# Optimization experiments

Measured on AMD Instinct MI355X. Metric: run time of the kernel, lower is better.

Reference implementation:

```python
import jax, jax.numpy as jnp
import numpy as np
from jax.lax import associative_scan

D_H = 512

def _binary_operator(e_i, e_j):
    a_i, kv_i = e_i
    a_j, kv_j = e_j
    return (a_j * a_i, a_j * kv_i + kv_j)

def setup_inputs() -> dict:
    key = jax.random.key(0)
    x = jax.random.normal(key, (4, 8192, 3 * D_H), dtype=jnp.float32)
    return {"x": x}

def reference(x):
    d_h = x.shape[-1] // 3
    inp = jnp.tanh(x[:, :, :d_h])
    gates = jax.nn.sigmoid(x[:, :, d_h:])
    input_gate, output_gate = jnp.split(gates, 2, axis=-1)
    forget_gate = 1.0 - input_gate
    # diagonal linear recurrence h_t = f_t * h_{t-1} + i_t * x_t via associative scan
    _, hidden_state = associative_scan(_binary_operator, (forget_gate, inp * input_gate), axis=1)
    return jnp.tanh(hidden_state) * output_gate
```

## Files before the change

kernel.cpp:

```cpp
#include <hip/hip_runtime.h>


#define B_    4
#define T_    8192
#define DH_   512
#define ROW4_ 384
#define DG4_  128
#define C_    512
#define TC_   (T_ / C_)

typedef float nat4 __attribute__((ext_vector_type(4)));

__device__ __forceinline__ float sigmoid_f(float x) {
    return __fdividef(1.0f, 1.0f + __expf(-x));
}
__device__ __forceinline__ float tanh_f(float x) {
    return 1.0f - __fdividef(2.0f, __expf(2.0f * x) + 1.0f);
}

__device__ __forceinline__ void step_agg(float xv, float gv, float& A, float& K) {
    const float s  = sigmoid_f(gv);
    const float f  = 1.0f - s;
    A = f * A;
    K = f * K + tanh_f(xv) * s;
}

__global__ __launch_bounds__(128) void k_partials(
        const float4* __restrict__ x4,
        float4* __restrict__ aggA,
        float4* __restrict__ aggKV) {
    const int c  = blockIdx.x;
    const int b  = blockIdx.y;
    const int d4 = threadIdx.x;
    const float4* xb = x4 + (size_t)b * T_ * ROW4_;
    const int t0 = c * TC_;

    float4 A  = make_float4(1.0f, 1.0f, 1.0f, 1.0f);
    float4 KV = make_float4(0.0f, 0.0f, 0.0f, 0.0f);
#pragma unroll 4
    for (int i = 0; i < TC_; ++i) {
        const size_t r = (size_t)(t0 + i) * ROW4_ + d4;
        const float4 xi = xb[r];
        const float4 gi = xb[r + DG4_];
        step_agg(xi.x, gi.x, A.x, KV.x);
        step_agg(xi.y, gi.y, A.y, KV.y);
        step_agg(xi.z, gi.z, A.z, KV.z);
        step_agg(xi.w, gi.w, A.w, KV.w);
    }
    const size_t idx = ((size_t)b * C_ + c) * DG4_ + d4;
    aggA[idx]  = A;
    aggKV[idx] = KV;
}

__global__ __launch_bounds__(128) void k_scan(
        const float4* __restrict__ aggA,
        const float4* __restrict__ aggKV,
        float4* __restrict__ pref) {
    const int b  = blockIdx.x;
    const int d4 = threadIdx.x;

    float4 h = make_float4(0.0f, 0.0f, 0.0f, 0.0f);
    for (int c = 0; c < C_; ++c) {
        const size_t idx = ((size_t)b * C_ + c) * DG4_ + d4;
        pref[idx] = h;
        const float4 a  = aggA[idx];
        const float4 kv = aggKV[idx];
        h.x = a.x * h.x + kv.x;
        h.y = a.y * h.y + kv.y;
        h.z = a.z * h.z + kv.z;
        h.w = a.w * h.w + kv.w;
    }
}

__global__ __launch_bounds__(128) void k_apply(
        const float4* __restrict__ x4,
        const float4* __restrict__ pref,
        float4* __restrict__ out4) {
    const int c  = blockIdx.x;
    const int b  = blockIdx.y;
    const int d4 = threadIdx.x;

    float4 h = pref[((size_t)b * C_ + c) * DG4_ + d4];

    const float4* xb = x4 + (size_t)b * T_ * ROW4_;
    float4* ob = out4 + (size_t)b * T_ * DG4_;
    const int t0 = c * TC_;

#pragma unroll 4
    for (int i = 0; i < TC_; ++i) {
        const size_t r = (size_t)(t0 + i) * ROW4_ + d4;
        const float4 xi = xb[r];
        const float4 gi = xb[r + DG4_];
        const float4 go = xb[r + 2 * DG4_];
        float4 o;
        {
            const float s = sigmoid_f(gi.x), f = 1.0f - s;
            h.x = f * h.x + tanh_f(xi.x) * s;
            o.x = tanh_f(h.x) * sigmoid_f(go.x);
        }
        {
            const float s = sigmoid_f(gi.y), f = 1.0f - s;
            h.y = f * h.y + tanh_f(xi.y) * s;
            o.y = tanh_f(h.y) * sigmoid_f(go.y);
        }
        {
            const float s = sigmoid_f(gi.z), f = 1.0f - s;
            h.z = f * h.z + tanh_f(xi.z) * s;
            o.z = tanh_f(h.z) * sigmoid_f(go.z);
        }
        {
            const float s = sigmoid_f(gi.w), f = 1.0f - s;
            h.w = f * h.w + tanh_f(xi.w) * s;
            o.w = tanh_f(h.w) * sigmoid_f(go.w);
        }
        nat4 ov = {o.x, o.y, o.z, o.w};
        __builtin_nontemporal_store(ov, (nat4*)&ob[(size_t)(t0 + i) * DG4_ + d4]);
    }
}

extern "C" void kernel_launch(void* const* d_in, const int* in_sizes, int n_in,
                              void* d_out, int out_size, void* d_ws, size_t ws_size,
                              hipStream_t stream) {
    const float4* x4 = (const float4*)d_in[0];
    float4* out4 = (float4*)d_out;

    float4* aggA  = (float4*)d_ws;
    float4* aggKV = aggA  + (size_t)B_ * C_ * DG4_;
    float4* pref  = aggKV + (size_t)B_ * C_ * DG4_;

    hipLaunchKernelGGL(k_partials, dim3(C_, B_), dim3(128), 0, stream, x4, aggA, aggKV);
    hipLaunchKernelGGL(k_scan,     dim3(B_),     dim3(128), 0, stream, aggA, aggKV, pref);
    hipLaunchKernelGGL(k_apply,    dim3(C_, B_), dim3(128), 0, stream, x4, pref, out4);
}
```

Before: 363.2 us.

## Fuse three-pass chunked scan into one cooperative kernel with two-level prefix

Replaces the partials, serial scan and apply kernels with a single cooperative kernel using grid-wide syncs. Chunk count drops to 256, and the serial per-batch scan over all chunks becomes a two-level scheme: 32 groups scan their chunks locally, then each block combines the preceding group totals. The intent is to remove the long serial scan kernel and the launch gaps between kernels. In exchange it depends on co-residency of all 1024 blocks for grid sync, lowers parallelism per pass, and drops the nontemporal output store.

```diff
diff --git a/kernel.cpp b/kernel.cpp
--- a/kernel.cpp
+++ b/kernel.cpp
@@ -1,15 +1,17 @@
 #include <hip/hip_runtime.h>
+#include <hip/hip_cooperative_groups.h>
+
+namespace cg = cooperative_groups;
 
 
 #define B_    4
 #define T_    8192
-#define DH_   512
 #define ROW4_ 384
 #define DG4_  128
-#define C_    512
+#define C_    256
 #define TC_   (T_ / C_)
-
-typedef float nat4 __attribute__((ext_vector_type(4)));
+#define G_    32
+#define GS_   (C_ / G_)
 
 __device__ __forceinline__ float sigmoid_f(float x) {
     return __fdividef(1.0f, 1.0f + __expf(-x));
@@ -19,73 +21,90 @@
 }
 
 __device__ __forceinline__ void step_agg(float xv, float gv, float& A, float& K) {
-    const float s  = sigmoid_f(gv);
-    const float f  = 1.0f - s;
+    const float s = sigmoid_f(gv);
+    const float f = 1.0f - s;
     A = f * A;
     K = f * K + tanh_f(xv) * s;
 }
 
-__global__ __launch_bounds__(128) void k_partials(
+__device__ __forceinline__ void affine4(float4& h, const float4 a, const float4 kv) {
+    h.x = a.x * h.x + kv.x;
+    h.y = a.y * h.y + kv.y;
+    h.z = a.z * h.z + kv.z;
+    h.w = a.w * h.w + kv.w;
+}
+
+__global__ __launch_bounds__(128, 4) void scan_coop(
         const float4* __restrict__ x4,
+        float4* __restrict__ out4,
         float4* __restrict__ aggA,
-        float4* __restrict__ aggKV) {
+        float4* __restrict__ aggKV,
+        float4* __restrict__ locA,
+        float4* __restrict__ locKV,
+        float4* __restrict__ grpA,
+        float4* __restrict__ grpKV) {
     const int c  = blockIdx.x;
     const int b  = blockIdx.y;
     const int d4 = threadIdx.x;
     const float4* xb = x4 + (size_t)b * T_ * ROW4_;
     const int t0 = c * TC_;
+    cg::grid_group grid = cg::this_grid();
 
-    float4 A  = make_float4(1.0f, 1.0f, 1.0f, 1.0f);
-    float4 KV = make_float4(0.0f, 0.0f, 0.0f, 0.0f);
+    {
+        float4 A  = make_float4(1.0f, 1.0f, 1.0f, 1.0f);
+        float4 KV = make_float4(0.0f, 0.0f, 0.0f, 0.0f);
 #pragma unroll 4
-    for (int i = 0; i < TC_; ++i) {
-        const size_t r = (size_t)(t0 + i) * ROW4_ + d4;
-        const float4 xi = xb[r];
-        const float4 gi = xb[r + DG4_];
-        step_agg(xi.x, gi.x, A.x, KV.x);
-        step_agg(xi.y, gi.y, A.y, KV.y);
-        step_agg(xi.z, gi.z, A.z, KV.z);
-        step_agg(xi.w, gi.w, A.w, KV.w);
+        for (int i = 0; i < TC_; ++i) {
+            const size_t r = (size_t)(t0 + i) * ROW4_ + d4;
+            const float4 xi = xb[r];
+            const float4 gi = xb[r + DG4_];
+            step_agg(xi.x, gi.x, A.x, KV.x);
+            step_agg(xi.y, gi.y, A.y, KV.y);
+            step_agg(xi.z, gi.z, A.z, KV.z);
+            step_agg(xi.w, gi.w, A.w, KV.w);
+        }
+        const size_t idx = ((size_t)b * C_ + c) * DG4_ + d4;
+        aggA[idx]  = A;
+        aggKV[idx] = KV;
     }
-    const size_t idx = ((size_t)b * C_ + c) * DG4_ + d4;
-    aggA[idx]  = A;
-    aggKV[idx] = KV;
-}
 
-__global__ __launch_bounds__(128) void k_scan(
-        const float4* __restrict__ aggA,
-        const float4* __restrict__ aggKV,
-        float4* __restrict__ pref) {
-    const int b  = blockIdx.x;
-    const int d4 = threadIdx.x;
+    grid.sync();
 
+    if (c < G_) {
+        const int g = c;
+        float4 A  = make_float4(1.0f, 1.0f, 1.0f, 1.0f);
+        float4 KV = make_float4(0.0f, 0.0f, 0.0f, 0.0f);
+#pragma unroll
+        for (int j = 0; j < GS_; ++j) {
+            const size_t idx = ((size_t)b * C_ + g * GS_ + j) * DG4_ + d4;
+            locA[idx]  = A;
+            locKV[idx] = KV;
+            const float4 ca = aggA[idx];
+            const float4 ck = aggKV[idx];
+            A.x = ca.x * A.x;  KV.x = ca.x * KV.x + ck.x;
+            A.y = ca.y * A.y;  KV.y = ca.y * KV.y + ck.y;
+            A.z = ca.z * A.z;  KV.z = ca.z * KV.z + ck.z;
+            A.w = ca.w * A.w;  KV.w = ca.w * KV.w + ck.w;
+        }
+        const size_t gidx = ((size_t)b * G_ + g) * DG4_ + d4;
+        grpA[gidx]  = A;
+        grpKV[gidx] = KV;
+    }
+
+    grid.sync();
+
+    const int g = c / GS_;
     float4 h = make_float4(0.0f, 0.0f, 0.0f, 0.0f);
-    for (int c = 0; c < C_; ++c) {
+    for (int gg = 0; gg < g; ++gg) {
+        const size_t gidx = ((size_t)b * G_ + gg) * DG4_ + d4;
+        affine4(h, grpA[gidx], grpKV[gidx]);
+    }
+    {
         const size_t idx = ((size_t)b * C_ + c) * DG4_ + d4;
-        pref[idx] = h;
-        const float4 a  = aggA[idx];
-        const float4 kv = aggKV[idx];
-        h.x = a.x * h.x + kv.x;
-        h.y = a.y * h.y + kv.y;
-        h.z = a.z * h.z + kv.z;
-        h.w = a.w * h.w + kv.w;
+        affine4(h, locA[idx], locKV[idx]);
     }
-}
 
-__global__ __launch_bounds__(128) void k_apply(
-        const float4* __restrict__ x4,
-        const float4* __restrict__ pref,
-        float4* __restrict__ out4) {
-    const int c  = blockIdx.x;
-    const int b  = blockIdx.y;
-    const int d4 = threadIdx.x;
-
-    float4 h = pref[((size_t)b * C_ + c) * DG4_ + d4];
-
-    const float4* xb = x4 + (size_t)b * T_ * ROW4_;
     float4* ob = out4 + (size_t)b * T_ * DG4_;
-    const int t0 = c * TC_;
-
 #pragma unroll 4
     for (int i = 0; i < TC_; ++i) {
         const size_t r = (size_t)(t0 + i) * ROW4_ + d4;
@@ -113,8 +132,7 @@
             h.w = f * h.w + tanh_f(xi.w) * s;
             o.w = tanh_f(h.w) * sigmoid_f(go.w);
         }
-        nat4 ov = {o.x, o.y, o.z, o.w};
-        __builtin_nontemporal_store(ov, (nat4*)&ob[(size_t)(t0 + i) * DG4_ + d4]);
+        ob[(size_t)(t0 + i) * DG4_ + d4] = o;
     }
 }
 
@@ -124,11 +142,19 @@
     const float4* x4 = (const float4*)d_in[0];
     float4* out4 = (float4*)d_out;
 
+    const size_t NC = (size_t)B_ * C_ * DG4_;
+    const size_t NG = (size_t)B_ * G_ * DG4_;
     float4* aggA  = (float4*)d_ws;
-    float4* aggKV = aggA  + (size_t)B_ * C_ * DG4_;
-    float4* pref  = aggKV + (size_t)B_ * C_ * DG4_;
+    float4* aggKV = aggA  + NC;
+    float4* locA  = aggKV + NC;
+    float4* locKV = locA  + NC;
+    float4* grpA  = locKV + NC;
+    float4* grpKV = grpA  + NG;
 
-    hipLaunchKernelGGL(k_partials, dim3(C_, B_), dim3(128), 0, stream, x4, aggA, aggKV);
-    hipLaunchKernelGGL(k_scan,     dim3(B_),     dim3(128), 0, stream, aggA, aggKV, pref);
-    hipLaunchKernelGGL(k_apply,    dim3(C_, B_), dim3(128), 0, stream, x4, pref, out4);
+    void* args[] = { (void*)&x4, (void*)&out4,
+                     (void*)&aggA, (void*)&aggKV,
+                     (void*)&locA, (void*)&locKV,
+                     (void*)&grpA, (void*)&grpKV };
+    hipLaunchCooperativeKernel((const void*)scan_coop,
+                               dim3(C_, B_), dim3(128), args, 0, stream);
 }
```

Result: slower. 524.8 us (+44.5%).
